# Optimization experiments

Hardware: AMD Instinct MI355X
Metric: run time of the kernel (lower is better)

## Reference

```python
import jax, jax.numpy as jnp
import numpy as np


def setup_inputs() -> dict:
    key = jax.random.key(0)
    ks = jax.random.split(key, 8)
    B, C, H, W = 8, 64, 256, 256
    Cq = C // 8
    return {
        "x": jax.random.normal(ks[0], (B, C, H, W), dtype=jnp.float32),
        "Wq": jax.random.normal(ks[1], (Cq, C), dtype=jnp.float32) * 0.1,
        "bq": jax.random.normal(ks[2], (Cq,), dtype=jnp.float32) * 0.1,
        "Wk": jax.random.normal(ks[3], (Cq, C), dtype=jnp.float32) * 0.1,
        "bk": jax.random.normal(ks[4], (Cq,), dtype=jnp.float32) * 0.1,
        "Wv": jax.random.normal(ks[5], (C, C), dtype=jnp.float32) * 0.1,
        "bv": jax.random.normal(ks[6], (C,), dtype=jnp.float32) * 0.1,
        "gamma": jax.random.normal(ks[7], (1,), dtype=jnp.float32),
    }


def _criss_cross(x, Wq, bq, Wk, bk, Wv, bv, gamma):
    # 1x1 convs == per-pixel linear maps over channel dim
    q = jnp.einsum('bchw,oc->bohw', x, Wq) + bq[None, :, None, None]  # [B,Cq,H,W]
    k = jnp.einsum('bchw,oc->bohw', x, Wk) + bk[None, :, None, None]  # [B,Cq,H,W]
    v = jnp.einsum('bchw,oc->bohw', x, Wv) + bv[None, :, None, None]  # [B,C,H,W]

    # --- column (height) attention: independent per (b, w) ---
    # attn_h[b,w,i,j] = <q[:, :, i, w], k[:, :, j, w]>, softmax over j
    attn_h = jnp.einsum('bciw,bcjw->bwij', q, k)            # [B,W,H,H]
    attn_h = jax.nn.softmax(attn_h, axis=-1)
    # torch: h_out = bmm(value[BW,C,H], attn[BW,H,H]) -> out[c,j] = sum_i v[c,i]*attn[i,j]
    h_out = jnp.einsum('bciw,bwij->bcjw', v, attn_h)        # [B,C,H,W]

    # --- row (width) attention: independent per (b, h) ---
    attn_w = jnp.einsum('bchw,bchv->bhwv', q, k)            # [B,H,W,W]
    attn_w = jax.nn.softmax(attn_w, axis=-1)
    w_out = jnp.einsum('bchw,bhwv->bchv', v, attn_w)        # [B,C,H,W]

    return gamma[0] * (h_out + w_out) + x


def reference(x, Wq, bq, Wk, bk, Wv, bv, gamma):
    return _criss_cross(x, Wq, bq, Wk, bk, Wv, bv, gamma)
```

## Files before the change

kernel.cpp:

```cpp
#include <hip/hip_runtime.h>
#include <cstddef>

namespace {

constexpr int    Bn   = 8;
constexpr int    Cc   = 64;
constexpr int    Cq   = 8;
constexpr int    Ln   = 256;
constexpr size_t HWn  = 65536;
constexpr size_t NPIX = (size_t)Bn * HWn;
constexpr size_t VPLANE = NPIX * 16;

constexpr float LOG2E = 1.44269504088896f;

constexpr size_t WT_B = 0;
constexpr size_t QH_B = 32768;
constexpr size_t QL_B = QH_B + NPIX * 8 * 2;
constexpr size_t KH_B = QL_B + NPIX * 8 * 2;
constexpr size_t KL_B = KH_B + NPIX * 8 * 2;
constexpr size_t VB_B = KL_B + NPIX * 8 * 2;
constexpr size_t HO_B = VB_B + NPIX * 64 * 2;
constexpr size_t WO_B = HO_B + NPIX * 64 * 2;

typedef short bf16x8 __attribute__((ext_vector_type(8)));
typedef float f32x16 __attribute__((ext_vector_type(16)));
typedef unsigned short u16x4 __attribute__((ext_vector_type(4)));

__device__ __forceinline__ unsigned short f2bf(float x) {
  union { float f; unsigned u; } c; c.f = x;
  unsigned u = c.u + 0x7FFFu + ((c.u >> 16) & 1u);
  return (unsigned short)(u >> 16);
}
__device__ __forceinline__ float bf2f(unsigned short h) {
  union { unsigned u; float f; } c; c.u = ((unsigned)h) << 16;
  return c.f;
}
__device__ __forceinline__ float fast_exp2(float x) {
#if __has_builtin(__builtin_amdgcn_exp2f)
  return __builtin_amdgcn_exp2f(x);
#else
  float r;
  asm("v_exp_f32 %0, %1" : "=v"(r) : "v"(x));
  return r;
#endif
}
__device__ __forceinline__ f32x16 zero16() {
  f32x16 z;
#pragma unroll
  for (int i = 0; i < 16; ++i) z[i] = 0.f;
  return z;
}

}

__global__ void pack_weights(const float* __restrict__ Wq,
                             const float* __restrict__ Wk,
                             const float* __restrict__ Wv,
                             float* __restrict__ wt) {
  int idx = blockIdx.x * 256 + threadIdx.x;
  if (idx >= 64 * 80) return;
  int c = idx / 80, o = idx % 80;
  float v;
  if (o < 8)       v = Wq[o * 64 + c] * LOG2E;
  else if (o < 16) v = Wk[(o - 8) * 64 + c];
  else             v = Wv[(o - 16) * 64 + c];
  wt[idx] = v;
}

__global__ __launch_bounds__(256) void qkv_kernel(
    const float* __restrict__ x, const float* __restrict__ wt,
    const float* __restrict__ bq, const float* __restrict__ bk,
    const float* __restrict__ bv,
    unsigned short* __restrict__ qh, unsigned short* __restrict__ ql,
    unsigned short* __restrict__ kh, unsigned short* __restrict__ kl,
    unsigned short* __restrict__ vb) {
  const int d = blockIdx.x;
  const int lin = (d & 7) * 1280 + (d >> 3);
  const int chunk = lin % 5;
  size_t p = (size_t)(lin / 5) * 256 + threadIdx.x;
  int b = (int)(p >> 16);
  int rem = (int)(p & 65535);
  const float* xb = x + (size_t)b * 64 * HWn + rem;

  float acc[16];
  if (chunk == 0) {
#pragma unroll
    for (int o = 0; o < 8; ++o) { acc[o] = bq[o] * LOG2E; acc[8 + o] = bk[o]; }
  } else {
#pragma unroll
    for (int o = 0; o < 16; ++o) acc[o] = bv[(chunk - 1) * 16 + o];
  }
  const int woff = (chunk == 0) ? 0 : 16 + (chunk - 1) * 16;

#pragma unroll 1
  for (int c0 = 0; c0 < 64; c0 += 8) {
    float xv[8];
#pragma unroll
    for (int cc = 0; cc < 8; ++cc) xv[cc] = xb[(size_t)(c0 + cc) * HWn];
#pragma unroll
    for (int cc = 0; cc < 8; ++cc) {
      const float* w = wt + (c0 + cc) * 80 + woff;
      const float xc = xv[cc];
#pragma unroll
      for (int o = 0; o < 16; ++o) acc[o] = fmaf(xc, w[o], acc[o]);
    }
  }

  if (chunk == 0) {
    unsigned h8[16], l8[16];
#pragma unroll
    for (int o = 0; o < 16; ++o) {
      h8[o] = f2bf(acc[o]);
      l8[o] = f2bf(acc[o] - bf2f((unsigned short)h8[o]));
    }
    uint4 pqh = make_uint4(h8[0] | (h8[1] << 16), h8[2] | (h8[3] << 16),
                           h8[4] | (h8[5] << 16), h8[6] | (h8[7] << 16));
    uint4 pql = make_uint4(l8[0] | (l8[1] << 16), l8[2] | (l8[3] << 16),
                           l8[4] | (l8[5] << 16), l8[6] | (l8[7] << 16));
    uint4 pkh = make_uint4(h8[8] | (h8[9] << 16), h8[10] | (h8[11] << 16),
                           h8[12] | (h8[13] << 16), h8[14] | (h8[15] << 16));
    uint4 pkl = make_uint4(l8[8] | (l8[9] << 16), l8[10] | (l8[11] << 16),
                           l8[12] | (l8[13] << 16), l8[14] | (l8[15] << 16));
    *(uint4*)(qh + p * 8) = pqh;
    *(uint4*)(ql + p * 8) = pql;
    *(uint4*)(kh + p * 8) = pkh;
    *(uint4*)(kl + p * 8) = pkl;
  } else {
    unsigned e[16];
#pragma unroll
    for (int u = 0; u < 16; ++u) e[u] = f2bf(acc[u]);
    uint4 p0 = make_uint4(e[0] | (e[1] << 16), e[2] | (e[3] << 16),
                          e[4] | (e[5] << 16), e[6] | (e[7] << 16));
    uint4 p1 = make_uint4(e[8] | (e[9] << 16), e[10] | (e[11] << 16),
                          e[12] | (e[13] << 16), e[14] | (e[15] << 16));
    unsigned short* vp = vb + (size_t)(chunk - 1) * VPLANE + p * 16;
    *(uint4*)(vp + 0) = p0;
    *(uint4*)(vp + 8) = p1;
  }
}

template <int MODE>
__global__ __launch_bounds__(256) void attn_kernel(
    const unsigned short* __restrict__ qh, const unsigned short* __restrict__ ql,
    const unsigned short* __restrict__ kh, const unsigned short* __restrict__ kl,
    const unsigned short* __restrict__ vb, _Float16* __restrict__ o) {
  const int s = (MODE == 1) ? (((blockIdx.x & 7) << 8) | (blockIdx.x >> 3))
                            : blockIdx.x;
  const int t = threadIdx.x;
  const int b = s >> 8;
  const int r = s & 255;
  const int w = t >> 6;
  const int l = t & 63;
  const int g = l >> 5;
  const int ln = l & 31;

  __shared__ short qs_h[256 * 8], qs_l[256 * 8];
  __shared__ short ks_h[256 * 8], ks_l[256 * 8];
  __shared__ short vz[16384];
  __shared__ float Zl[256];

  size_t qkb, qk_stride;
  size_t v_pix_base, v_pix_stride;
  if (MODE == 0) {
    qkb    = (size_t)s * (Ln * Cq);  qk_stride = Cq;
    v_pix_base = (size_t)s * Ln;     v_pix_stride = 1;
  } else {
    qkb    = ((size_t)b * HWn + r) * Cq;  qk_stride = (size_t)Ln * Cq;
    v_pix_base = (size_t)b * HWn + r;     v_pix_stride = Ln;
  }

  {
    const size_t off = qkb + (size_t)t * qk_stride;
    *(bf16x8*)&qs_h[t * 8] = *(const bf16x8*)(qh + off);
    *(bf16x8*)&qs_l[t * 8] = *(const bf16x8*)(ql + off);
    *(bf16x8*)&ks_h[t * 8] = *(const bf16x8*)(kh + off);
    *(bf16x8*)&ks_l[t * 8] = *(const bf16x8*)(kl + off);
  }
  Zl[t] = 0.f;
  __syncthreads();

  {
    const short* kb = g ? ks_l : ks_h;
    bf16x8 afk0 = *(const bf16x8*)&kb[(ln + 32 * (2 * w + 0)) * 8];
    bf16x8 afk1 = *(const bf16x8*)&kb[(ln + 32 * (2 * w + 1)) * 8];
#pragma unroll 1
    for (int it = 0; it < 8; ++it) {
      int i = ln + 32 * it;
      bf16x8 bh = *(const bf16x8*)&qs_h[i * 8];
      bf16x8 bl = *(const bf16x8*)&qs_l[i * 8];
      float zp = 0.f;
      {
        f32x16 c = zero16();
        c = __builtin_amdgcn_mfma_f32_32x32x16_bf16(afk0, bh, c, 0, 0, 0);
        c = __builtin_amdgcn_mfma_f32_32x32x16_bf16(afk0, bl, c, 0, 0, 0);
#pragma unroll
        for (int rr = 0; rr < 16; ++rr) zp += fast_exp2(c[rr]);
      }
      {
        f32x16 c = zero16();
        c = __builtin_amdgcn_mfma_f32_32x32x16_bf16(afk1, bh, c, 0, 0, 0);
        c = __builtin_amdgcn_mfma_f32_32x32x16_bf16(afk1, bl, c, 0, 0, 0);
#pragma unroll
        for (int rr = 0; rr < 16; ++rr) zp += fast_exp2(c[rr]);
      }
      atomicAdd(&Zl[i], zp);
    }
  }
  __syncthreads();
  Zl[t] = 1.0f / Zl[t];
  __syncthreads();

#pragma unroll 1
  for (int rnd = 0; rnd < 16; ++rnd) {
    int idx = rnd * 256 + t;
    int i = idx >> 4;
    int c4 = (idx & 15) << 2;
    const unsigned short* vp = vb + (size_t)(c4 >> 4) * VPLANE +
                               (v_pix_base + (size_t)i * v_pix_stride) * 16 +
                               (c4 & 15);
    u16x4 raw = *(const u16x4*)vp;
    float iz = Zl[i];
    int sg = i >> 4, rem = i & 15;
    int a = rem >> 3, g2 = (rem >> 2) & 1, t0 = rem & 3;
    int e = 4 * a + t0;
#pragma unroll
    for (int u = 0; u < 4; ++u) {
      int c = c4 + u;
      int lane_s = 32 * g2 + (c & 31);
      int mt = c >> 5;
      vz[((sg * 2 + mt) * 64 + lane_s) * 8 + e] =
          (short)f2bf(bf2f(raw[u]) * iz);
    }
  }
  __syncthreads();

  f32x16 acc00 = zero16(), acc01 = zero16(), acc10 = zero16(), acc11 = zero16();
  {
    bf16x8 bkh[2], bkl[2];
#pragma unroll
    for (int nt2 = 0; nt2 < 2; ++nt2) {
      int j = ln + 32 * (2 * w + nt2);
      bkh[nt2] = *(const bf16x8*)&ks_h[j * 8];
      bkl[nt2] = *(const bf16x8*)&ks_l[j * 8];
    }
    const short* qb = g ? qs_l : qs_h;
#pragma unroll 1
    for (int it = 0; it < 8; ++it) {
      int i = ln + 32 * it;
      bf16x8 aQ = *(const bf16x8*)&qb[i * 8];
      bf16x8 pf[2][2];
#pragma unroll
      for (int nt2 = 0; nt2 < 2; ++nt2) {
        f32x16 c = zero16();
        c = __builtin_amdgcn_mfma_f32_32x32x16_bf16(aQ, bkh[nt2], c, 0, 0, 0);
        c = __builtin_amdgcn_mfma_f32_32x32x16_bf16(aQ, bkl[nt2], c, 0, 0, 0);
#pragma unroll
        for (int rr = 0; rr < 8; ++rr)
          pf[nt2][0][rr] = (short)f2bf(fast_exp2(c[rr]));
#pragma unroll
        for (int rr = 0; rr < 8; ++rr)
          pf[nt2][1][rr] = (short)f2bf(fast_exp2(c[8 + rr]));
      }
#pragma unroll
      for (int s2 = 0; s2 < 2; ++s2) {
#pragma unroll
        for (int mt = 0; mt < 2; ++mt) {
          bf16x8 vf = *(const bf16x8*)&vz[(((it * 2 + s2) * 2 + mt) * 64 + l) * 8];
          if (mt == 0) {
            acc00 = __builtin_amdgcn_mfma_f32_32x32x16_bf16(vf, pf[0][s2], acc00, 0, 0, 0);
            acc10 = __builtin_amdgcn_mfma_f32_32x32x16_bf16(vf, pf[1][s2], acc10, 0, 0, 0);
          } else {
            acc01 = __builtin_amdgcn_mfma_f32_32x32x16_bf16(vf, pf[0][s2], acc01, 0, 0, 0);
            acc11 = __builtin_amdgcn_mfma_f32_32x32x16_bf16(vf, pf[1][s2], acc11, 0, 0, 0);
          }
        }
      }
    }
  }

#pragma unroll
  for (int nt2 = 0; nt2 < 2; ++nt2) {
    int j = ln + 32 * (2 * w + nt2);
#pragma unroll
    for (int mt = 0; mt < 2; ++mt) {
      const f32x16& A = (nt2 == 0) ? (mt == 0 ? acc00 : acc01)
                                   : (mt == 0 ? acc10 : acc11);
#pragma unroll
      for (int reg = 0; reg < 16; ++reg) {
        int c = (reg & 3) + 8 * (reg >> 2) + 4 * g + 32 * mt;
        if (MODE == 0) {
          o[((size_t)b * 64 + c) * HWn + (size_t)r * 256 + j] = (_Float16)A[reg];
        } else {
          o[((size_t)s * 64 + c) * 256 + j] = (_Float16)A[reg];
        }
      }
    }
  }
}

__global__ __launch_bounds__(256) void merge_kernel(
    const _Float16* __restrict__ wo, const _Float16* __restrict__ ho,
    const float* __restrict__ x, const float* __restrict__ gamma,
    float* __restrict__ out) {
  const int h0 = blockIdx.x * 64;
  const int c = blockIdx.y;
  const int b = blockIdx.z;
  const int t = threadIdx.x;
  __shared__ _Float16 lds[256 * 66];

  const float g = gamma[0];

#pragma unroll
  for (int it = 0; it < 8; ++it) {
    int e = it * 256 + t;
    int w = e >> 3, q8 = (e & 7) << 3;
    uint4 f = *(const uint4*)&ho[(((size_t)b * 256 + w) * 64 + c) * 256 + h0 + q8];
    unsigned* dst = (unsigned*)&lds[w * 66 + q8];
    dst[0] = f.x; dst[1] = f.y; dst[2] = f.z; dst[3] = f.w;
  }
  __syncthreads();

#pragma unroll 4
  for (int rr = 0; rr < 64; ++rr) {
    size_t idx = (((size_t)b * 64 + c) * 256 + h0 + rr) * 256 + t;
    out[idx] = g * ((float)wo[idx] + (float)lds[t * 66 + rr]) + x[idx];
  }
}

extern "C" void kernel_launch(void* const* d_in, const int* in_sizes, int n_in,
                              void* d_out, int out_size, void* d_ws, size_t ws_size,
                              hipStream_t stream) {
  const float* x     = (const float*)d_in[0];
  const float* Wq    = (const float*)d_in[1];
  const float* bq    = (const float*)d_in[2];
  const float* Wk    = (const float*)d_in[3];
  const float* bk    = (const float*)d_in[4];
  const float* Wv    = (const float*)d_in[5];
  const float* bv    = (const float*)d_in[6];
  const float* gamma = (const float*)d_in[7];
  float* out = (float*)d_out;
  char*  ws  = (char*)d_ws;

  float*          wt = (float*)(ws + WT_B);
  unsigned short* qh = (unsigned short*)(ws + QH_B);
  unsigned short* ql = (unsigned short*)(ws + QL_B);
  unsigned short* kh = (unsigned short*)(ws + KH_B);
  unsigned short* kl = (unsigned short*)(ws + KL_B);
  unsigned short* vb = (unsigned short*)(ws + VB_B);
  _Float16*       ho = (_Float16*)(ws + HO_B);
  _Float16*       wo = (_Float16*)(ws + WO_B);

  hipLaunchKernelGGL(pack_weights, dim3(20), dim3(256), 0, stream, Wq, Wk, Wv, wt);
  hipLaunchKernelGGL(qkv_kernel, dim3(10240), dim3(256), 0, stream,
                     x, wt, bq, bk, bv, qh, ql, kh, kl, vb);
  hipLaunchKernelGGL((attn_kernel<0>), dim3(2048), dim3(256), 0, stream,
                     qh, ql, kh, kl, vb, wo);
  hipLaunchKernelGGL((attn_kernel<1>), dim3(2048), dim3(256), 0, stream,
                     qh, ql, kh, kl, vb, ho);
  hipLaunchKernelGGL(merge_kernel, dim3(4, 64, 8), dim3(256), 0, stream,
                     wo, ho, x, gamma, out);
}
```

Before: 504.3 us.

## Use hardware bf16 pack converts, double-buffer x loads, and drop LDS atomics

Replaces the software round-to-nearest bf16 conversion with the v_cvt_pk_bf16_f32 instruction in the QKV projection, the V staging and the softmax probability packing. The QKV loop now prefetches the next group of eight channels of x while the current group is being used, so load latency overlaps with the FMAs. The softmax denominator is no longer built with LDS atomicAdd: each wave and half-wave writes its partial sums to a scratch area aliased onto the vz buffer, and a reduction pass sums them. The V staging loop also has its index arithmetic hoisted out of the loop. This cuts ALU work and contention in several stages, at the cost of an inline-asm dependency and reusing vz before it is filled.

```diff
diff --git a/kernel.cpp b/kernel.cpp
--- a/kernel.cpp
+++ b/kernel.cpp
@@ -26,14 +26,17 @@
 typedef float f32x16 __attribute__((ext_vector_type(16)));
 typedef unsigned short u16x4 __attribute__((ext_vector_type(4)));
 
-__device__ __forceinline__ unsigned short f2bf(float x) {
-  union { float f; unsigned u; } c; c.f = x;
-  unsigned u = c.u + 0x7FFFu + ((c.u >> 16) & 1u);
-  return (unsigned short)(u >> 16);
-}
 __device__ __forceinline__ float bf2f(unsigned short h) {
   union { unsigned u; float f; } c; c.u = ((unsigned)h) << 16;
   return c.f;
+}
+__device__ __forceinline__ float fbits(unsigned u) {
+  union { unsigned u; float f; } c; c.u = u; return c.f;
+}
+__device__ __forceinline__ unsigned cvt_pk_bf16(float a, float b) {
+  unsigned r;
+  asm("v_cvt_pk_bf16_f32 %0, %1, %2" : "=v"(r) : "v"(a), "v"(b));
+  return r;
 }
 __device__ __forceinline__ float fast_exp2(float x) {
 #if __has_builtin(__builtin_amdgcn_exp2f)
@@ -80,7 +83,7 @@
   size_t p = (size_t)(lin / 5) * 256 + threadIdx.x;
   int b = (int)(p >> 16);
   int rem = (int)(p & 65535);
-  const float* xb = x + (size_t)b * 64 * HWn + rem;
+  const float* xbase = x + (size_t)b * 64 * HWn + rem;
 
   float acc[16];
   if (chunk == 0) {
@@ -92,50 +95,53 @@
   }
   const int woff = (chunk == 0) ? 0 : 16 + (chunk - 1) * 16;
 
+  float xa[8], xn[8];
+#pragma unroll
+  for (int cc = 0; cc < 8; ++cc) xa[cc] = xbase[(size_t)cc * HWn];
+
 #pragma unroll 1
-  for (int c0 = 0; c0 < 64; c0 += 8) {
-    float xv[8];
-#pragma unroll
-    for (int cc = 0; cc < 8; ++cc) xv[cc] = xb[(size_t)(c0 + cc) * HWn];
+  for (int c0 = 0; c0 < 64; c0 += 16) {
+#pragma unroll
+    for (int cc = 0; cc < 8; ++cc) xn[cc] = xbase[(size_t)(c0 + 8 + cc) * HWn];
 #pragma unroll
     for (int cc = 0; cc < 8; ++cc) {
       const float* w = wt + (c0 + cc) * 80 + woff;
-      const float xc = xv[cc];
+      const float xc = xa[cc];
 #pragma unroll
       for (int o = 0; o < 16; ++o) acc[o] = fmaf(xc, w[o], acc[o]);
     }
+    const int cnx = (c0 + 16) & 63;
+#pragma unroll
+    for (int cc = 0; cc < 8; ++cc) xa[cc] = xbase[(size_t)(cnx + cc) * HWn];
+#pragma unroll
+    for (int cc = 0; cc < 8; ++cc) {
+      const float* w = wt + (c0 + 8 + cc) * 80 + woff;
+      const float xc = xn[cc];
+#pragma unroll
+      for (int o = 0; o < 16; ++o) acc[o] = fmaf(xc, w[o], acc[o]);
+    }
   }
 
   if (chunk == 0) {
-    unsigned h8[16], l8[16];
-#pragma unroll
-    for (int o = 0; o < 16; ++o) {
-      h8[o] = f2bf(acc[o]);
-      l8[o] = f2bf(acc[o] - bf2f((unsigned short)h8[o]));
-    }
-    uint4 pqh = make_uint4(h8[0] | (h8[1] << 16), h8[2] | (h8[3] << 16),
-                           h8[4] | (h8[5] << 16), h8[6] | (h8[7] << 16));
-    uint4 pql = make_uint4(l8[0] | (l8[1] << 16), l8[2] | (l8[3] << 16),
-                           l8[4] | (l8[5] << 16), l8[6] | (l8[7] << 16));
-    uint4 pkh = make_uint4(h8[8] | (h8[9] << 16), h8[10] | (h8[11] << 16),
-                           h8[12] | (h8[13] << 16), h8[14] | (h8[15] << 16));
-    uint4 pkl = make_uint4(l8[8] | (l8[9] << 16), l8[10] | (l8[11] << 16),
-                           l8[12] | (l8[13] << 16), l8[14] | (l8[15] << 16));
-    *(uint4*)(qh + p * 8) = pqh;
-    *(uint4*)(ql + p * 8) = pql;
-    *(uint4*)(kh + p * 8) = pkh;
-    *(uint4*)(kl + p * 8) = pkl;
+    unsigned dh[8], dl[8];
+#pragma unroll
+    for (int k = 0; k < 8; ++k) {
+      float a0 = acc[2 * k], a1 = acc[2 * k + 1];
+      unsigned h = cvt_pk_bf16(a0, a1);
+      dl[k] = cvt_pk_bf16(a0 - fbits(h << 16), a1 - fbits(h & 0xffff0000u));
+      dh[k] = h;
+    }
+    *(uint4*)(qh + p * 8) = make_uint4(dh[0], dh[1], dh[2], dh[3]);
+    *(uint4*)(ql + p * 8) = make_uint4(dl[0], dl[1], dl[2], dl[3]);
+    *(uint4*)(kh + p * 8) = make_uint4(dh[4], dh[5], dh[6], dh[7]);
+    *(uint4*)(kl + p * 8) = make_uint4(dl[4], dl[5], dl[6], dl[7]);
   } else {
-    unsigned e[16];
-#pragma unroll
-    for (int u = 0; u < 16; ++u) e[u] = f2bf(acc[u]);
-    uint4 p0 = make_uint4(e[0] | (e[1] << 16), e[2] | (e[3] << 16),
-                          e[4] | (e[5] << 16), e[6] | (e[7] << 16));
-    uint4 p1 = make_uint4(e[8] | (e[9] << 16), e[10] | (e[11] << 16),
-                          e[12] | (e[13] << 16), e[14] | (e[15] << 16));
+    unsigned dv[8];
+#pragma unroll
+    for (int k = 0; k < 8; ++k) dv[k] = cvt_pk_bf16(acc[2 * k], acc[2 * k + 1]);
     unsigned short* vp = vb + (size_t)(chunk - 1) * VPLANE + p * 16;
-    *(uint4*)(vp + 0) = p0;
-    *(uint4*)(vp + 8) = p1;
+    *(uint4*)(vp + 0) = make_uint4(dv[0], dv[1], dv[2], dv[3]);
+    *(uint4*)(vp + 8) = make_uint4(dv[4], dv[5], dv[6], dv[7]);
   }
 }
 
@@ -159,6 +165,8 @@
   __shared__ short vz[16384];
   __shared__ float Zl[256];
 
+  float* Zp = (float*)vz;
+
   size_t qkb, qk_stride;
   size_t v_pix_base, v_pix_stride;
   if (MODE == 0) {
@@ -176,11 +184,11 @@
     *(bf16x8*)&ks_h[t * 8] = *(const bf16x8*)(kh + off);
     *(bf16x8*)&ks_l[t * 8] = *(const bf16x8*)(kl + off);
   }
-  Zl[t] = 0.f;
   __syncthreads();
 
   {
     const short* kb = g ? ks_l : ks_h;
+    const int wg = (w << 1) | g;
     bf16x8 afk0 = *(const bf16x8*)&kb[(ln + 32 * (2 * w + 0)) * 8];
     bf16x8 afk1 = *(const bf16x8*)&kb[(ln + 32 * (2 * w + 1)) * 8];
 #pragma unroll 1
@@ -188,48 +196,63 @@
       int i = ln + 32 * it;
       bf16x8 bh = *(const bf16x8*)&qs_h[i * 8];
       bf16x8 bl = *(const bf16x8*)&qs_l[i * 8];
-      float zp = 0.f;
+      float z0 = 0.f, z1 = 0.f, z2 = 0.f, z3 = 0.f;
       {
         f32x16 c = zero16();
         c = __builtin_amdgcn_mfma_f32_32x32x16_bf16(afk0, bh, c, 0, 0, 0);
         c = __builtin_amdgcn_mfma_f32_32x32x16_bf16(afk0, bl, c, 0, 0, 0);
 #pragma unroll
-        for (int rr = 0; rr < 16; ++rr) zp += fast_exp2(c[rr]);
+        for (int rr = 0; rr < 16; ++rr) {
+          float e = fast_exp2(c[rr]);
+          if ((rr & 3) == 0) z0 += e; else if ((rr & 3) == 1) z1 += e;
+          else if ((rr & 3) == 2) z2 += e; else z3 += e;
+        }
       }
       {
         f32x16 c = zero16();
         c = __builtin_amdgcn_mfma_f32_32x32x16_bf16(afk1, bh, c, 0, 0, 0);
         c = __builtin_amdgcn_mfma_f32_32x32x16_bf16(afk1, bl, c, 0, 0, 0);
 #pragma unroll
-        for (int rr = 0; rr < 16; ++rr) zp += fast_exp2(c[rr]);
-      }
-      atomicAdd(&Zl[i], zp);
-    }
-  }
-  __syncthreads();
-  Zl[t] = 1.0f / Zl[t];
-  __syncthreads();
-
+        for (int rr = 0; rr < 16; ++rr) {
+          float e = fast_exp2(c[rr]);
+          if ((rr & 3) == 0) z0 += e; else if ((rr & 3) == 1) z1 += e;
+          else if ((rr & 3) == 2) z2 += e; else z3 += e;
+        }
+      }
+      Zp[(wg << 8) + i] = (z0 + z1) + (z2 + z3);
+    }
+  }
+  __syncthreads();
+  {
+    float z = 0.f;
+#pragma unroll
+    for (int k = 0; k < 8; ++k) z += Zp[(k << 8) + t];
+    Zl[t] = 1.0f / z;
+  }
+  __syncthreads();
+
+  {
+    const int rem_i = t >> 4;
+    const int c4 = (t & 15) << 2;
+    const int a = rem_i >> 3, g2 = (rem_i >> 2) & 1, t0 = rem_i & 3;
+    const int e = 4 * a + t0;
+    const int mt = c4 >> 5;
+    const int lane_s0 = 32 * g2 + (c4 & 31);
+    short* vz0 = &vz[(mt * 64 + lane_s0) * 8 + e];
+    const unsigned short* vp0 = vb + (size_t)(c4 >> 4) * VPLANE +
+                                (v_pix_base + (size_t)rem_i * v_pix_stride) * 16 +
+                                (c4 & 15);
+    const size_t step = (size_t)256 * v_pix_stride;
 #pragma unroll 1
-  for (int rnd = 0; rnd < 16; ++rnd) {
-    int idx = rnd * 256 + t;
-    int i = idx >> 4;
-    int c4 = (idx & 15) << 2;
-    const unsigned short* vp = vb + (size_t)(c4 >> 4) * VPLANE +
-                               (v_pix_base + (size_t)i * v_pix_stride) * 16 +
-                               (c4 & 15);
-    u16x4 raw = *(const u16x4*)vp;
-    float iz = Zl[i];
-    int sg = i >> 4, rem = i & 15;
-    int a = rem >> 3, g2 = (rem >> 2) & 1, t0 = rem & 3;
-    int e = 4 * a + t0;
-#pragma unroll
-    for (int u = 0; u < 4; ++u) {
-      int c = c4 + u;
-      int lane_s = 32 * g2 + (c & 31);
-      int mt = c >> 5;
-      vz[((sg * 2 + mt) * 64 + lane_s) * 8 + e] =
-          (short)f2bf(bf2f(raw[u]) * iz);
+    for (int rnd = 0; rnd < 16; ++rnd) {
+      u16x4 raw = *(const u16x4*)vp0;
+      float iz = Zl[(rnd << 4) + rem_i];
+#pragma unroll
+      for (int u = 0; u < 4; ++u) {
+        unsigned dd = cvt_pk_bf16(bf2f(raw[u]) * iz, 0.f);
+        vz0[rnd * 1024 + u * 8] = (short)dd;
+      }
+      vp0 += step;
     }
   }
   __syncthreads();
@@ -254,12 +277,15 @@
         f32x16 c = zero16();
         c = __builtin_amdgcn_mfma_f32_32x32x16_bf16(aQ, bkh[nt2], c, 0, 0, 0);
         c = __builtin_amdgcn_mfma_f32_32x32x16_bf16(aQ, bkl[nt2], c, 0, 0, 0);
-#pragma unroll
-        for (int rr = 0; rr < 8; ++rr)
-          pf[nt2][0][rr] = (short)f2bf(fast_exp2(c[rr]));
-#pragma unroll
-        for (int rr = 0; rr < 8; ++rr)
-          pf[nt2][1][rr] = (short)f2bf(fast_exp2(c[8 + rr]));
+        union { unsigned u[4]; bf16x8 v; } cv0, cv1;
+#pragma unroll
+        for (int k = 0; k < 4; ++k)
+          cv0.u[k] = cvt_pk_bf16(fast_exp2(c[2 * k]), fast_exp2(c[2 * k + 1]));
+#pragma unroll
+        for (int k = 0; k < 4; ++k)
+          cv1.u[k] = cvt_pk_bf16(fast_exp2(c[8 + 2 * k]), fast_exp2(c[8 + 2 * k + 1]));
+        pf[nt2][0] = cv0.v;
+        pf[nt2][1] = cv1.v;
       }
 #pragma unroll
       for (int s2 = 0; s2 < 2; ++s2) {
```

New measurement: 472.2 us. -6.4%, faster.
